# Kernel optimization log

Hardware: AMD Instinct MI355X
Metric: run time of the kernel (lower is better)

Reference implementation:

```python
import jax, jax.numpy as jnp
import numpy as np

TAU = 0.7
N_NODES = 1024
N_EDGES = 32768

def _mlp3(x, W1, b1, W2, b2, W3, b3):
    h = jax.nn.relu(x @ W1 + b1)
    h = jax.nn.relu(h @ W2 + b2)
    return h @ W3 + b3

def _gcn_conv(x, src, dst, W, b, n):
    # PyG GCNConv(add_self_loops=False): out = D^-1/2 A D^-1/2 (x W) + b
    deg = jax.ops.segment_sum(jnp.ones(src.shape[0], x.dtype), dst, num_segments=n)
    dinv = jnp.where(deg > 0, jax.lax.rsqrt(jnp.maximum(deg, 1.0)), 0.0)
    h = x @ W
    msg = h[src] * (dinv[src] * dinv[dst])[:, None]
    return jax.ops.segment_sum(msg, dst, num_segments=n) + b

def _forward(x1, x11, x2, mlp_W1, mlp_b1, mlp_W2, mlp_b2, mlp_W3, mlp_b3,
             m1_W1, m1_b1, m1_W2, m1_b2, m1_W3, m1_b3,
             wm1, bp1, bp2, wm12, wm13, class2,
             gcn1_W, gcn1_b, wm2, gcn2_W, gcn2_b, fc_W, fc_b, src, dst):
    n = x1.shape[0]
    logits = _mlp3(x1, mlp_W1, mlp_b1, mlp_W2, mlp_b2, mlp_W3, mlp_b3)  # [N,3]
    g = _mlp3(x11, m1_W1, m1_b1, m1_W2, m1_b2, m1_W3, m1_b3)            # [N,2]
    # hard argmax routing, softened: tau at argmax, (1-tau)/2 at the 2 others
    oh = jax.nn.one_hot(jnp.argmax(logits, axis=1), 3, dtype=logits.dtype)
    r = oh * TAU + (1.0 - oh) * ((1.0 - TAU) * 0.5)                     # [N,3]
    # fused form of: (einsum('nj,jkl',g,class2) * x2[...,None]).sum(-1) + g@b1
    res1 = jnp.einsum('nj,jkl,nk->nk', g, class2, x2) + g @ bp1         # [N,768]
    # fused form of: (einsum('nj,jkl',r,wm1) * res1[...,None]).sum(-1) + r@b2
    res1 = jnp.einsum('nj,jkl,nk->nk', r, wm1, res1) + r @ bp2          # [N,768]
    h1 = jax.nn.relu(_gcn_conv(res1, src, dst, gcn1_W, gcn1_b, n))      # [N,256]
    h1 = (r @ wm12) * h1 + 2e-4 * (res1 @ wm13)                         # [N,256]
    res2 = jnp.einsum('nj,jkl,nk->nk', r, wm2, h1)                      # [N,256]
    h2 = jax.nn.relu(_gcn_conv(res2, src, dst, gcn2_W, gcn2_b, n))      # [N,32]
    return jax.nn.log_softmax(h2 @ fc_W + fc_b, axis=1)                 # [N,8]

def setup_inputs():
    key = jax.random.key(0)
    ks = jax.random.split(key, 32)
    f = jnp.float32
    nrm = lambda i, s, sc=0.05: sc * jax.random.normal(ks[i], s, f)
    return {
        'x1': nrm(0, (N_NODES, 768), 1.0),
        'x11': nrm(1, (N_NODES, 768), 1.0),
        'x2': nrm(2, (N_NODES, 768), 1.0),
        'mlp_W1': nrm(3, (768, 512)), 'mlp_b1': jnp.zeros((512,), f),
        'mlp_W2': nrm(4, (512, 512)), 'mlp_b2': jnp.zeros((512,), f),
        'mlp_W3': nrm(5, (512, 3)), 'mlp_b3': jnp.zeros((3,), f),
        'm1_W1': nrm(6, (768, 512)), 'm1_b1': jnp.zeros((512,), f),
        'm1_W2': nrm(7, (512, 512)), 'm1_b2': jnp.zeros((512,), f),
        'm1_W3': nrm(8, (512, 2)), 'm1_b3': jnp.zeros((2,), f),
        'wm1': nrm(9, (3, 768, 256)),
        'bp1': jnp.zeros((2, 768), f),
        'bp2': jnp.zeros((3, 768), f),
        'wm12': jnp.ones((3, 256), f),
        'wm13': nrm(10, (768, 256)),
        'class2': jnp.ones((2, 768, 64), f),
        'gcn1_W': nrm(11, (768, 256)), 'gcn1_b': jnp.zeros((256,), f),
        'wm2': nrm(12, (3, 256, 256)),
        'gcn2_W': nrm(13, (256, 32)), 'gcn2_b': jnp.zeros((32,), f),
        'fc_W': nrm(14, (32, 8)), 'fc_b': jnp.zeros((8,), f),
        'edge_index': jax.random.randint(ks[15], (2, N_EDGES), 0, N_NODES),
    }

def reference(x1, x11, x2, mlp_W1, mlp_b1, mlp_W2, mlp_b2, mlp_W3, mlp_b3,
              m1_W1, m1_b1, m1_W2, m1_b2, m1_W3, m1_b3,
              wm1, bp1, bp2, wm12, wm13, class2,
              gcn1_W, gcn1_b, wm2, gcn2_W, gcn2_b, fc_W, fc_b, edge_index):
    src, dst = edge_index[0], edge_index[1]
    return _forward(x1, x11, x2, mlp_W1, mlp_b1, mlp_W2, mlp_b2, mlp_W3, mlp_b3,
                    m1_W1, m1_b1, m1_W2, m1_b2, m1_W3, m1_b3,
                    wm1, bp1, bp2, wm12, wm13, class2,
                    gcn1_W, gcn1_b, wm2, gcn2_W, gcn2_b, fc_W, fc_b, src, dst)
```

## Files before the change

kernel.cpp:

```cpp
#include <hip/hip_runtime.h>
#include <hip/hip_bf16.h>

#define NN 1024
#define NE 32768
#define TAU 0.7f
#define GAPT 0.01f

typedef __attribute__((ext_vector_type(8))) short short8;
typedef __attribute__((ext_vector_type(4))) float f32x4;

__device__ inline ushort bf16rne(float x) {
    union { float f; unsigned u; } a; a.f = x;
    unsigned r = (a.u + 0x7FFFu + ((a.u >> 16) & 1u)) >> 16;
    return (ushort)r;
}
__device__ inline float bf16tof(ushort h) {
    union { unsigned u; float f; } a; a.u = ((unsigned)h) << 16;
    return a.f;
}
__device__ inline void bf16split(float x, ushort& h, ushort& l) {
    h = bf16rne(x);
    l = bf16rne(x - bf16tof(h));
}

template <int K, int EPI>
__device__ __forceinline__ void gemm_wave(
    int lane, int rt, int ct,
    const ushort* __restrict__ Ah, const ushort* __restrict__ Al,
    const ushort* __restrict__ Bh, const ushort* __restrict__ Bl,
    const float* __restrict__ bias, const float* __restrict__ W3,
    float* __restrict__ Cf, ushort* __restrict__ Oh, ushort* __restrict__ Ol, int N) {
    int r0 = rt * 16, c0 = ct * 32;
    int g = lane >> 4, q = lane & 15;
    const ushort* pah = Ah + (size_t)(r0 + q) * K + g * 8;
    const ushort* pal = Al + (size_t)(r0 + q) * K + g * 8;
    const ushort* pb0h = Bh + (size_t)(c0 + q) * K + g * 8;
    const ushort* pb0l = Bl + (size_t)(c0 + q) * K + g * 8;
    const ushort* pb1h = pb0h + (size_t)16 * K;
    const ushort* pb1l = pb0l + (size_t)16 * K;
    f32x4 acc0 = {0.f, 0.f, 0.f, 0.f};
    f32x4 acc1 = {0.f, 0.f, 0.f, 0.f};
#pragma unroll 2
    for (int k0 = 0; k0 < K; k0 += 32) {
        short8 ah = *(const short8*)(pah + k0);
        short8 al = *(const short8*)(pal + k0);
        short8 b0h = *(const short8*)(pb0h + k0);
        short8 b0l = *(const short8*)(pb0l + k0);
        short8 b1h = *(const short8*)(pb1h + k0);
        short8 b1l = *(const short8*)(pb1l + k0);
        acc0 = __builtin_amdgcn_mfma_f32_16x16x32_bf16(ah, b0h, acc0, 0, 0, 0);
        acc1 = __builtin_amdgcn_mfma_f32_16x16x32_bf16(ah, b1h, acc1, 0, 0, 0);
        acc0 = __builtin_amdgcn_mfma_f32_16x16x32_bf16(ah, b0l, acc0, 0, 0, 0);
        acc1 = __builtin_amdgcn_mfma_f32_16x16x32_bf16(ah, b1l, acc1, 0, 0, 0);
        acc0 = __builtin_amdgcn_mfma_f32_16x16x32_bf16(al, b0h, acc0, 0, 0, 0);
        acc1 = __builtin_amdgcn_mfma_f32_16x16x32_bf16(al, b1h, acc1, 0, 0, 0);
    }
    int col0 = c0 + q, col1 = c0 + 16 + q;
    if constexpr (EPI == 0) {
#pragma unroll
        for (int i = 0; i < 4; i++) {
            int row = r0 + g * 4 + i;
            Cf[(size_t)row * N + col0] = acc0[i];
            Cf[(size_t)row * N + col1] = acc1[i];
        }
    } else if constexpr (EPI == 1) {
        float bv0 = bias[col0], bv1 = bias[col1];
#pragma unroll
        for (int i = 0; i < 4; i++) {
            int row = r0 + g * 4 + i;
            float a0 = fmaxf(acc0[i] + bv0, 0.f);
            float a1 = fmaxf(acc1[i] + bv1, 0.f);
            ushort h, l;
            bf16split(a0, h, l);
            Oh[(size_t)row * N + col0] = h;
            Ol[(size_t)row * N + col0] = l;
            bf16split(a1, h, l);
            Oh[(size_t)row * N + col1] = h;
            Ol[(size_t)row * N + col1] = l;
        }
    } else {
        constexpr int J = (EPI == 2) ? 3 : 2;
        constexpr int STR = (EPI == 2) ? 4 : 2;
        float bv0 = bias[col0], bv1 = bias[col1];
        float s[4][J];
#pragma unroll
        for (int i = 0; i < 4; i++) {
            float a0 = fmaxf(acc0[i] + bv0, 0.f);
            float a1 = fmaxf(acc1[i] + bv1, 0.f);
#pragma unroll
            for (int j = 0; j < J; j++)
                s[i][j] = a0 * W3[col0 * J + j] + a1 * W3[col1 * J + j];
        }
#pragma unroll
        for (int i = 0; i < 4; i++)
#pragma unroll
            for (int j = 0; j < J; j++) {
                float v = s[i][j];
#pragma unroll
                for (int m = 1; m < 16; m <<= 1) v += __shfl_xor(v, m);
                s[i][j] = v;
            }
        if (q == 0) {
#pragma unroll
            for (int i = 0; i < 4; i++) {
                int row = r0 + g * 4 + i;
#pragma unroll
                for (int j = 0; j < J; j++) atomicAdd(&Cf[(size_t)row * STR + j], s[i][j]);
            }
        }
    }
}

template <int M, int N, int K>
__global__ __launch_bounds__(256) void gemm3_n16(
    const ushort* __restrict__ Ah, const ushort* __restrict__ Al,
    const ushort* __restrict__ Bh, const ushort* __restrict__ Bl,
    float* __restrict__ Cf) {
    constexpr int RT = M / 16;
    constexpr int JOBS = RT * (N / 16);
    int wid = (blockIdx.x * 256 + threadIdx.x) >> 6;
    if (wid >= JOBS) return;
    int lane = threadIdx.x & 63;
    int rt = wid % RT, ct = wid / RT;
    int r0 = rt * 16, c0 = ct * 16;
    int g = lane >> 4, q = lane & 15;
    const ushort* pah = Ah + (size_t)(r0 + q) * K + g * 8;
    const ushort* pal = Al + (size_t)(r0 + q) * K + g * 8;
    const ushort* pbh = Bh + (size_t)(c0 + q) * K + g * 8;
    const ushort* pbl = Bl + (size_t)(c0 + q) * K + g * 8;
    f32x4 acc = {0.f, 0.f, 0.f, 0.f};
#pragma unroll 2
    for (int k0 = 0; k0 < K; k0 += 32) {
        short8 ah = *(const short8*)(pah + k0);
        short8 al = *(const short8*)(pal + k0);
        short8 bh = *(const short8*)(pbh + k0);
        short8 bl = *(const short8*)(pbl + k0);
        acc = __builtin_amdgcn_mfma_f32_16x16x32_bf16(ah, bh, acc, 0, 0, 0);
        acc = __builtin_amdgcn_mfma_f32_16x16x32_bf16(ah, bl, acc, 0, 0, 0);
        acc = __builtin_amdgcn_mfma_f32_16x16x32_bf16(al, bh, acc, 0, 0, 0);
    }
    int col = c0 + q;
#pragma unroll
    for (int i = 0; i < 4; i++) {
        int row = r0 + g * 4 + i;
        Cf[(size_t)row * N + col] = acc[i];
    }
}

template <int K, int EPI0, int EPI1, int RIDER>
__global__ __launch_bounds__(256) void gemm_pair(
    const ushort* __restrict__ Ah0, const ushort* __restrict__ Al0,
    const ushort* __restrict__ Bh0, const ushort* __restrict__ Bl0,
    const float* __restrict__ bias0, const float* __restrict__ W30,
    float* __restrict__ Cf0, ushort* __restrict__ Oh0, ushort* __restrict__ Ol0,
    const ushort* __restrict__ Ah1, const ushort* __restrict__ Al1,
    const ushort* __restrict__ Bh1, const ushort* __restrict__ Bl1,
    const float* __restrict__ bias1, const float* __restrict__ W31,
    float* __restrict__ Cf1, ushort* __restrict__ Oh1, ushort* __restrict__ Ol1,
    const int* __restrict__ esrc, const int* __restrict__ edst,
    const int* __restrict__ part, int* __restrict__ rowst, int* __restrict__ cursor,
    float* __restrict__ dinv, int* __restrict__ adj) {
    if (RIDER == 1 && blockIdx.x >= 512) {
        __shared__ int ps[256];
        int t = threadIdx.x;
        int d0 = 0, d1 = 0, d2 = 0, d3 = 0;
#pragma unroll
        for (int b = 0; b < 8; b++) {
            int4 qv = *(const int4*)(part + b * 1024 + t * 4);
            d0 += qv.x; d1 += qv.y; d2 += qv.z; d3 += qv.w;
        }
        int sum = d0 + d1 + d2 + d3;
        ps[t] = sum;
        __syncthreads();
        for (int off = 1; off < 256; off <<= 1) {
            int v = (t >= off) ? ps[t - off] : 0;
            __syncthreads();
            ps[t] += v;
            __syncthreads();
        }
        int r0 = ps[t] - sum;
        int r1 = r0 + d0, r2 = r1 + d1, r3 = r2 + d2;
        rowst[t * 4 + 0] = r0;
        rowst[t * 4 + 1] = r1;
        rowst[t * 4 + 2] = r2;
        rowst[t * 4 + 3] = r3;
        if (t == 255) rowst[1024] = r3 + d3;
        cursor[t * 4 + 0] = r0;
        cursor[t * 4 + 1] = r1;
        cursor[t * 4 + 2] = r2;
        cursor[t * 4 + 3] = r3;
        dinv[t * 4 + 0] = d0 > 0 ? rsqrtf((float)d0) : 0.f;
        dinv[t * 4 + 1] = d1 > 0 ? rsqrtf((float)d1) : 0.f;
        dinv[t * 4 + 2] = d2 > 0 ? rsqrtf((float)d2) : 0.f;
        dinv[t * 4 + 3] = d3 > 0 ? rsqrtf((float)d3) : 0.f;
        return;
    }
    if (RIDER == 2 && blockIdx.x >= 512) {
        int e = (blockIdx.x - 512) * 256 + threadIdx.x;
        int d = edst[e];
        int slot = atomicAdd(&cursor[d], 1);
        adj[slot] = esrc[e];
        return;
    }
    int wid = (blockIdx.x * 256 + threadIdx.x) >> 6;
    int lane = threadIdx.x & 63;
    int pair = wid >> 10;
    int widl = wid & 1023;
    int rt = widl & 63, ct = widl >> 6;
    if (pair == 0)
        gemm_wave<K, EPI0>(lane, rt, ct, Ah0, Al0, Bh0, Bl0, bias0, W30, Cf0, Oh0, Ol0, 512);
    else
        gemm_wave<K, EPI1>(lane, rt, ct, Ah1, Al1, Bh1, Bl1, bias1, W31, Cf1, Oh1, Ol1, 512);
}

__device__ void dev_zero(int sub, int t, float* zbase) {
    for (int i = sub * 256 + t; i < 6144; i += 512) zbase[i] = 0.f;
}

__device__ void dev_tabs_wave(int gw, int lane, const float* __restrict__ class2,
                              const float* __restrict__ wm1, const float* __restrict__ wm2,
                              float* __restrict__ C2s, float* __restrict__ Wm1s,
                              float* __restrict__ Wm2s) {
    if (gw < 2304) {
        float4 v = *(const float4*)(wm1 + (size_t)gw * 256 + lane * 4);
        float s = v.x + v.y + v.z + v.w;
#pragma unroll
        for (int m = 32; m; m >>= 1) s += __shfl_xor(s, m);
        if (lane == 0) Wm1s[gw] = s;
    } else if (gw < 3072) {
        int j = gw - 2304;
        float4 v = *(const float4*)(wm2 + (size_t)j * 256 + lane * 4);
        float s = v.x + v.y + v.z + v.w;
#pragma unroll
        for (int m = 32; m; m >>= 1) s += __shfl_xor(s, m);
        if (lane == 0) Wm2s[j] = s;
    } else {
        int row = (gw - 3072) * 4 + (lane >> 4);
        float4 v = *(const float4*)(class2 + (size_t)row * 64 + (lane & 15) * 4);
        float s = v.x + v.y + v.z + v.w;
#pragma unroll
        for (int m = 8; m; m >>= 1) s += __shfl_xor(s, m);
        if ((lane & 15) == 0) C2s[row] = s;
    }
}

__device__ void dev_splitx(int sub, int t, const float* __restrict__ X,
                           ushort* __restrict__ Xh, ushort* __restrict__ Xl) {
    int j = sub * 256 + t;
    float4 v = ((const float4*)X)[j];
    ushort h0, l0, h1, l1, h2, l2, h3, l3;
    bf16split(v.x, h0, l0);
    bf16split(v.y, h1, l1);
    bf16split(v.z, h2, l2);
    bf16split(v.w, h3, l3);
    ((ushort4*)Xh)[j] = make_ushort4(h0, h1, h2, h3);
    ((ushort4*)Xl)[j] = make_ushort4(l0, l1, l2, l3);
}

__global__ __launch_bounds__(1024) void aux0(
    const float* class2, const float* wm1, const float* wm2,
    float* C2s, float* Wm1s, float* Wm2s, float* zbase,
    const float* x1, ushort* XH1, ushort* XL1,
    const float* x11, ushort* XH2, ushort* XL2,
    const float* W1a, ushort* W1AH, ushort* W1AL,
    const float* W1b, ushort* W1BH, ushort* W1BL,
    const float* W2a, ushort* W2AH, ushort* W2AL,
    const float* W2b, ushort* W2BH, ushort* W2BL,
    const float* G1W, ushort* GWH, ushort* GWL,
    const float* W13, const int* edst, int* part) {
    if (blockIdx.x >= 1017) {
        __shared__ int hist[1024];
        int b = blockIdx.x - 1017;
        int t = threadIdx.x;
        hist[t] = 0;
        __syncthreads();
        const int* ep = edst + b * 4096;
#pragma unroll
        for (int i = 0; i < 4; i++) atomicAdd(&hist[ep[t + i * 1024]], 1);
        __syncthreads();
        part[b * 1024 + t] = hist[t];
        return;
    }
    __shared__ float tb[4][32][33];
    int quad = threadIdx.x >> 8;
    int t = threadIdx.x & 255;
    int sub = blockIdx.x * 4 + quad;
    if (sub >= 4066) return;
    const float* W = nullptr;
    ushort *Th = nullptr, *Tl = nullptr;
    int K = 0, N = 0, tile = 0;
    if (sub >= 3874)      { W = W13; Th = GWH + 256 * 768; Tl = GWL + 256 * 768; K = 768; N = 256; tile = sub - 3874; }
    else if (sub >= 3682) { W = G1W; Th = GWH; Tl = GWL; K = 768; N = 256; tile = sub - 3682; }
    else if (sub >= 3426) { W = W2b; Th = W2BH; Tl = W2BL; K = 512; N = 512; tile = sub - 3426; }
    else if (sub >= 3170) { W = W2a; Th = W2AH; Tl = W2AL; K = 512; N = 512; tile = sub - 3170; }
    else if (sub >= 2786) { W = W1b; Th = W1BH; Tl = W1BL; K = 768; N = 512; tile = sub - 2786; }
    else if (sub >= 2402) { W = W1a; Th = W1AH; Tl = W1AL; K = 768; N = 512; tile = sub - 2402; }
    int k0 = 0, n0 = 0;
    if (W) {
        k0 = (tile % (K / 32)) * 32;
        n0 = (tile / (K / 32)) * 32;
        int tx = t % 32, ty = t / 32;
        for (int i = ty; i < 32; i += 8)
            tb[quad][i][tx] = W[(size_t)(k0 + i) * N + n0 + tx];
    } else if (sub < 2) dev_zero(sub, t, zbase);
    else if (sub < 866) dev_tabs_wave((sub - 2) * 4 + (t >> 6), t & 63,
                                      class2, wm1, wm2, C2s, Wm1s, Wm2s);
    else if (sub < 1634) dev_splitx(sub - 866, t, x1, XH1, XL1);
    else dev_splitx(sub - 1634, t, x11, XH2, XL2);
    __syncthreads();
    if (W) {
        int tx = t % 32, ty = t / 32;
        for (int i = ty; i < 32; i += 8) {
            float v = tb[quad][tx][i];
            ushort h, l;
            bf16split(v, h, l);
            Th[(size_t)(n0 + i) * K + k0 + tx] = h;
            Tl[(size_t)(n0 + i) * K + k0 + tx] = l;
        }
    }
}

__global__ __launch_bounds__(256) void finrep(
    const float* __restrict__ LG, const float* __restrict__ b3, float* __restrict__ rbuf,
    const float* __restrict__ x1, const float* __restrict__ W1, const float* __restrict__ b1,
    const float* __restrict__ W2, const float* __restrict__ b2, const float* __restrict__ W3) {
    __shared__ int snode[4];
    __shared__ int scnt;
    __shared__ float part[4][512];
    __shared__ float xs[768];
    __shared__ float h1[512];
    __shared__ float h2[512];
    int t = threadIdx.x;
    if (t == 0) scnt = 0;
    __syncthreads();
    if (t < 4) {
        int n = blockIdx.x * 4 + t;
        float l0 = LG[n * 4 + 0] + b3[0];
        float l1 = LG[n * 4 + 1] + b3[1];
        float l2 = LG[n * 4 + 2] + b3[2];
        int am = 0;
        float mv = l0;
        if (l1 > mv) { mv = l1; am = 1; }
        if (l2 > mv) { mv = l2; am = 2; }
        float sec = (am == 0) ? fmaxf(l1, l2) : ((am == 1) ? fmaxf(l0, l2) : fmaxf(l0, l1));
        float lo = (1.f - TAU) * 0.5f;
        rbuf[n * 4 + 0] = (am == 0) ? TAU : lo;
        rbuf[n * 4 + 1] = (am == 1) ? TAU : lo;
        rbuf[n * 4 + 2] = (am == 2) ? TAU : lo;
        if (mv - sec < GAPT) {
            int s = atomicAdd(&scnt, 1);
            snode[s] = n;
        }
    }
    __syncthreads();
    int cnt = scnt;
    int w = t >> 6, l = t & 63;
    for (int it = 0; it < cnt; it++) {
        int n = snode[it];
        for (int k = t; k < 768; k += 256) xs[k] = x1[(size_t)n * 768 + k];
        __syncthreads();
        {
            float acc[8] = {0.f, 0.f, 0.f, 0.f, 0.f, 0.f, 0.f, 0.f};
            for (int k = w * 192; k < (w + 1) * 192; k++) {
                float xv = xs[k];
                const float* wr = W1 + (size_t)k * 512 + l;
#pragma unroll
                for (int c = 0; c < 8; c++) acc[c] += xv * wr[64 * c];
            }
#pragma unroll
            for (int c = 0; c < 8; c++) part[w][l + 64 * c] = acc[c];
        }
        __syncthreads();
        for (int d = t; d < 512; d += 256)
            h1[d] = fmaxf(part[0][d] + part[1][d] + part[2][d] + part[3][d] + b1[d], 0.f);
        __syncthreads();
        {
            float acc[8] = {0.f, 0.f, 0.f, 0.f, 0.f, 0.f, 0.f, 0.f};
            for (int k = w * 128; k < (w + 1) * 128; k++) {
                float xv = h1[k];
                const float* wr = W2 + (size_t)k * 512 + l;
#pragma unroll
                for (int c = 0; c < 8; c++) acc[c] += xv * wr[64 * c];
            }
#pragma unroll
            for (int c = 0; c < 8; c++) part[w][l + 64 * c] = acc[c];
        }
        __syncthreads();
        for (int d = t; d < 512; d += 256)
            h2[d] = fmaxf(part[0][d] + part[1][d] + part[2][d] + part[3][d] + b2[d], 0.f);
        __syncthreads();
        if (t < 64) {
            float p0 = 0.f, p1 = 0.f, p2 = 0.f;
            for (int k = t; k < 512; k += 64) {
                float hv = h2[k];
                p0 += hv * W3[k * 3 + 0];
                p1 += hv * W3[k * 3 + 1];
                p2 += hv * W3[k * 3 + 2];
            }
            for (int off = 32; off; off >>= 1) {
                p0 += __shfl_down(p0, off);
                p1 += __shfl_down(p1, off);
                p2 += __shfl_down(p2, off);
            }
            if (t == 0) {
                float l0 = p0 + b3[0], l1 = p1 + b3[1], l2 = p2 + b3[2];
                int am = 0;
                float mv = l0;
                if (l1 > mv) { mv = l1; am = 1; }
                if (l2 > mv) { mv = l2; am = 2; }
                float lo = (1.f - TAU) * 0.5f;
                rbuf[n * 4 + 0] = (am == 0) ? TAU : lo;
                rbuf[n * 4 + 1] = (am == 1) ? TAU : lo;
                rbuf[n * 4 + 2] = (am == 2) ? TAU : lo;
            }
        }
        __syncthreads();
    }
}

__global__ __launch_bounds__(256) void res1_kernel(
    const float* __restrict__ x2, const float* __restrict__ G, const float* __restrict__ m1b3,
    const float* __restrict__ rbuf, const float* __restrict__ C2s, const float* __restrict__ bp1,
    const float* __restrict__ Wm1s, const float* __restrict__ bp2,
    ushort* __restrict__ r1h, ushort* __restrict__ r1l) {
    int idx = blockIdx.x * 256 + threadIdx.x;
    int n = idx / 192;
    int kq = (idx % 192) * 4;
    float g0 = G[n * 2 + 0] + m1b3[0], g1 = G[n * 2 + 1] + m1b3[1];
    float r0 = rbuf[n * 4 + 0], r1 = rbuf[n * 4 + 1], r2 = rbuf[n * 4 + 2];
    float4 xv = *(const float4*)(x2 + (size_t)n * 768 + kq);
    float4 c0 = *(const float4*)(C2s + kq);
    float4 c1 = *(const float4*)(C2s + 768 + kq);
    float4 p0 = *(const float4*)(bp1 + kq);
    float4 p1 = *(const float4*)(bp1 + 768 + kq);
    float4 w0 = *(const float4*)(Wm1s + kq);
    float4 w1 = *(const float4*)(Wm1s + 768 + kq);
    float4 w2 = *(const float4*)(Wm1s + 1536 + kq);
    float4 q0 = *(const float4*)(bp2 + kq);
    float4 q1 = *(const float4*)(bp2 + 768 + kq);
    float4 q2 = *(const float4*)(bp2 + 1536 + kq);
    float o[4];
    o[0] = (xv.x * (g0 * c0.x + g1 * c1.x) + g0 * p0.x + g1 * p1.x) * (r0 * w0.x + r1 * w1.x + r2 * w2.x) + r0 * q0.x + r1 * q1.x + r2 * q2.x;
    o[1] = (xv.y * (g0 * c0.y + g1 * c1.y) + g0 * p0.y + g1 * p1.y) * (r0 * w0.y + r1 * w1.y + r2 * w2.y) + r0 * q0.y + r1 * q1.y + r2 * q2.y;
    o[2] = (xv.z * (g0 * c0.z + g1 * c1.z) + g0 * p0.z + g1 * p1.z) * (r0 * w0.z + r1 * w1.z + r2 * w2.z) + r0 * q0.z + r1 * q1.z + r2 * q2.z;
    o[3] = (xv.w * (g0 * c0.w + g1 * c1.w) + g0 * p0.w + g1 * p1.w) * (r0 * w0.w + r1 * w1.w + r2 * w2.w) + r0 * q0.w + r1 * q1.w + r2 * q2.w;
    ushort h[4], l[4];
#pragma unroll
    for (int i = 0; i < 4; i++) bf16split(o[i], h[i], l[i]);
    size_t off = ((size_t)n * 768 + kq) / 4;
    ((ushort4*)r1h)[off] = make_ushort4(h[0], h[1], h[2], h[3]);
    ((ushort4*)r1l)[off] = make_ushort4(l[0], l[1], l[2], l[3]);
}

__global__ __launch_bounds__(256) void gather1_combine(
    const float* __restrict__ gcw, const int* __restrict__ rowst, const int* __restrict__ adj,
    const float* __restrict__ dinv, const float* __restrict__ gcn1_b,
    const float* __restrict__ rbuf, const float* __restrict__ wm12,
    const float* __restrict__ Wm2s, float* __restrict__ res2f) {
    int n = blockIdx.x;
    int k = threadIdx.x;
    int lane = threadIdx.x & 63;
    int e0 = rowst[n], e1 = rowst[n + 1];
    float acc = 0.f;
    for (int base = e0; base < e1; base += 64) {
        int idx = base + lane;
        int s_i = 0;
        float w_i = 0.f;
        if (idx < e1) { s_i = adj[idx]; w_i = dinv[s_i]; }
        int mm = min(64, e1 - base);
        for (int j = 0; j < mm; j++) {
            int s = __shfl(s_i, j);
            float w = __shfl(w_i, j);
            acc += gcw[(size_t)s * 512 + k] * w;
        }
    }
    float h1 = dinv[n] * acc + gcn1_b[k];
    float mv = gcw[(size_t)n * 512 + 256 + k];
    float r0 = rbuf[n * 4 + 0], r1 = rbuf[n * 4 + 1], r2 = rbuf[n * 4 + 2];
    float a = r0 * wm12[k] + r1 * wm12[256 + k] + r2 * wm12[512 + k];
    float w = r0 * Wm2s[k] + r1 * Wm2s[256 + k] + r2 * Wm2s[512 + k];
    res2f[(size_t)n * 256 + k] = w * (a * fmaxf(h1, 0.f) + 2e-4f * mv);
}

__global__ __launch_bounds__(256) void gather2_full(
    const float* __restrict__ res2f, const int* __restrict__ rowst,
    const int* __restrict__ adj, const float* __restrict__ dinv,
    const float* __restrict__ G2W, const float* __restrict__ gcn2_b,
    const float* __restrict__ fcW, const float* __restrict__ fcb,
    float* __restrict__ out) {
    __shared__ float gres[256];
    __shared__ float part[8][32];
    int t = threadIdx.x;
    int lane = t & 63;
    int n = blockIdx.x;
    int e0 = rowst[n], e1 = rowst[n + 1];
    float acc = 0.f;
    for (int base = e0; base < e1; base += 64) {
        int idx = base + lane;
        int s_i = 0;
        float w_i = 0.f;
        if (idx < e1) { s_i = adj[idx]; w_i = dinv[s_i]; }
        int mm = min(64, e1 - base);
        for (int j = 0; j < mm; j++) {
            int s = __shfl(s_i, j);
            float w = __shfl(w_i, j);
            acc += res2f[(size_t)s * 256 + t] * w;
        }
    }
    gres[t] = acc * dinv[n];
    __syncthreads();
    int j = t & 31, seg = t >> 5;
    float p = 0.f;
#pragma unroll
    for (int kk = 0; kk < 32; kk++) {
        int k = seg * 32 + kk;
        p += gres[k] * G2W[k * 32 + j];
    }
    part[seg][j] = p;
    __syncthreads();
    if (t < 32) {
        float h2 = part[0][t] + part[1][t] + part[2][t] + part[3][t] +
                   part[4][t] + part[5][t] + part[6][t] + part[7][t] + gcn2_b[t];
        gres[t] = fmaxf(h2, 0.f);
    }
    __syncthreads();
    if (t < 8) {
        float logit = fcb[t];
#pragma unroll
        for (int i = 0; i < 32; i++) logit += gres[i] * fcW[i * 8 + t];
        float m = logit;
        for (int off = 4; off; off >>= 1) m = fmaxf(m, __shfl_xor(m, off, 8));
        float e = expf(logit - m), s = e;
        for (int off = 4; off; off >>= 1) s += __shfl_xor(s, off, 8);
        out[(size_t)n * 8 + t] = logit - m - logf(s);
    }
}

extern "C" void kernel_launch(void* const* d_in, const int* in_sizes, int n_in,
                              void* d_out, int out_size, void* d_ws, size_t ws_size,
                              hipStream_t stream) {
    const float* x1     = (const float*)d_in[0];
    const float* x11    = (const float*)d_in[1];
    const float* x2     = (const float*)d_in[2];
    const float* mlp_W1 = (const float*)d_in[3];
    const float* mlp_b1 = (const float*)d_in[4];
    const float* mlp_W2 = (const float*)d_in[5];
    const float* mlp_b2 = (const float*)d_in[6];
    const float* mlp_W3 = (const float*)d_in[7];
    const float* mlp_b3 = (const float*)d_in[8];
    const float* m1_W1  = (const float*)d_in[9];
    const float* m1_b1  = (const float*)d_in[10];
    const float* m1_W2  = (const float*)d_in[11];
    const float* m1_b2  = (const float*)d_in[12];
    const float* m1_W3  = (const float*)d_in[13];
    const float* m1_b3  = (const float*)d_in[14];
    const float* wm1    = (const float*)d_in[15];
    const float* bp1    = (const float*)d_in[16];
    const float* bp2    = (const float*)d_in[17];
    const float* wm12   = (const float*)d_in[18];
    const float* wm13   = (const float*)d_in[19];
    const float* class2 = (const float*)d_in[20];
    const float* gcn1_W = (const float*)d_in[21];
    const float* gcn1_b = (const float*)d_in[22];
    const float* wm2    = (const float*)d_in[23];
    const float* gcn2_W = (const float*)d_in[24];
    const float* gcn2_b = (const float*)d_in[25];
    const float* fc_W   = (const float*)d_in[26];
    const float* fc_b   = (const float*)d_in[27];
    const int* eidx     = (const int*)d_in[28];
    const int* esrc = eidx;
    const int* edst = eidx + NE;

    char* ws = (char*)d_ws;
    ushort* XH1   = (ushort*)(ws + 0x0000000);
    ushort* XL1   = (ushort*)(ws + 0x0180000);
    ushort* XH2   = (ushort*)(ws + 0x0300000);
    ushort* XL2   = (ushort*)(ws + 0x0480000);
    ushort* W1AH  = (ushort*)(ws + 0x0600000);
    ushort* W1AL  = (ushort*)(ws + 0x06C0000);
    ushort* W1BH  = (ushort*)(ws + 0x0780000);
    ushort* W1BL  = (ushort*)(ws + 0x0840000);
    ushort* W2AH  = (ushort*)(ws + 0x0900000);
    ushort* W2AL  = (ushort*)(ws + 0x0980000);
    ushort* W2BH  = (ushort*)(ws + 0x0A00000);
    ushort* W2BL  = (ushort*)(ws + 0x0A80000);
    ushort* GWH   = (ushort*)(ws + 0x0B00000);
    ushort* GWL   = (ushort*)(ws + 0x0BC0000);
    ushort* HS1AH = (ushort*)(ws + 0x0D00000);
    ushort* HS1AL = (ushort*)(ws + 0x0E00000);
    ushort* HS1BH = (ushort*)(ws + 0x0F00000);
    ushort* HS1BL = (ushort*)(ws + 0x1000000);
    ushort* RES1H = (ushort*)(ws + 0x1100000);
    ushort* RES1L = (ushort*)(ws + 0x1280000);
    float*  GCW   = (float*)(ws + 0x1400000);
    float*  RES2F = (float*)(ws + 0x1600000);
    float* LOGITS = (float*)(ws + 0x1740000);
    float* GBUF   = (float*)(ws + 0x1744000);
    float* RBUF   = (float*)(ws + 0x1746000);
    float* DINV   = (float*)(ws + 0x174A000);
    int*   ROWST  = (int*)(ws + 0x174B000);
    int*   CURS   = (int*)(ws + 0x174D000);
    int*   ADJ    = (int*)(ws + 0x174E000);
    int*   PART   = (int*)(ws + 0x1780000);
    float* C2S    = (float*)(ws + 0x1770000);
    float* WM1S   = (float*)(ws + 0x1772000);
    float* WM2S   = (float*)(ws + 0x1775000);

    aux0<<<1025, 1024, 0, stream>>>(class2, wm1, wm2, C2S, WM1S, WM2S, LOGITS,
                                    x1, XH1, XL1, x11, XH2, XL2,
                                    mlp_W1, W1AH, W1AL, m1_W1, W1BH, W1BL,
                                    mlp_W2, W2AH, W2AL, m1_W2, W2BH, W2BL,
                                    gcn1_W, GWH, GWL, wm13, edst, PART);
    gemm_pair<768, 1, 1, 1><<<513, 256, 0, stream>>>(
        XH1, XL1, W1AH, W1AL, mlp_b1, nullptr, nullptr, HS1AH, HS1AL,
        XH2, XL2, W1BH, W1BL, m1_b1, nullptr, nullptr, HS1BH, HS1BL,
        esrc, edst, PART, ROWST, CURS, DINV, ADJ);
    gemm_pair<512, 2, 3, 2><<<640, 256, 0, stream>>>(
        HS1AH, HS1AL, W2AH, W2AL, mlp_b2, mlp_W3, LOGITS, nullptr, nullptr,
        HS1BH, HS1BL, W2BH, W2BL, m1_b2, m1_W3, GBUF, nullptr, nullptr,
        esrc, edst, PART, ROWST, CURS, DINV, ADJ);
    finrep<<<256, 256, 0, stream>>>(LOGITS, mlp_b3, RBUF, x1, mlp_W1, mlp_b1,
                                    mlp_W2, mlp_b2, mlp_W3);
    res1_kernel<<<768, 256, 0, stream>>>(x2, GBUF, m1_b3, RBUF, C2S, bp1, WM1S, bp2,
                                         RES1H, RES1L);
    gemm3_n16<1024, 512, 768><<<512, 256, 0, stream>>>(RES1H, RES1L, GWH, GWL, GCW);
    gather1_combine<<<NN, 256, 0, stream>>>(GCW, ROWST, ADJ, DINV, gcn1_b, RBUF,
                                            wm12, WM2S, RES2F);
    gather2_full<<<NN, 256, 0, stream>>>(RES2F, ROWST, ADJ, DINV, gcn2_W, gcn2_b,
                                         fc_W, fc_b, (float*)d_out);
}
```

Measured before the change: 165.4 us.

## Fuse tail stages into one cooperative kernel with grid-wide syncs

The four tail launches (res1, the split-bf16 GEMM, and the two GCN gathers) become one cooperative persistent kernel whose phases are separated by grid syncs. The goal is to remove per-launch overhead and the idle gaps between the dependent small kernels. In exchange, the GEMM phase is a simpler per-wave MFMA loop that reads operands straight from global memory instead of the templated gemm3_n16, and the grid is capped by occupancy, which could leave parallelism unused. The old launch sequence stays as a fallback if the cooperative launch fails.

```diff
diff --git a/kernel.cpp b/kernel.cpp
--- a/kernel.cpp
+++ b/kernel.cpp
@@ -1,5 +1,8 @@
 #include <hip/hip_runtime.h>
 #include <hip/hip_bf16.h>
+#include <hip/hip_cooperative_groups.h>
+
+namespace cg = cooperative_groups;
 
 #define NN 1024
 #define NE 32768
@@ -418,12 +421,12 @@
     }
 }
 
-__global__ __launch_bounds__(256) void res1_kernel(
-    const float* __restrict__ x2, const float* __restrict__ G, const float* __restrict__ m1b3,
-    const float* __restrict__ rbuf, const float* __restrict__ C2s, const float* __restrict__ bp1,
+__device__ __forceinline__ void res1_body(
+    int idx, const float* __restrict__ x2, const float* __restrict__ G,
+    const float* __restrict__ m1b3, const float* __restrict__ rbuf,
+    const float* __restrict__ C2s, const float* __restrict__ bp1,
     const float* __restrict__ Wm1s, const float* __restrict__ bp2,
     ushort* __restrict__ r1h, ushort* __restrict__ r1l) {
-    int idx = blockIdx.x * 256 + threadIdx.x;
     int n = idx / 192;
     int kq = (idx % 192) * 4;
     float g0 = G[n * 2 + 0] + m1b3[0], g1 = G[n * 2 + 1] + m1b3[1];
@@ -444,22 +447,30 @@
     o[1] = (xv.y * (g0 * c0.y + g1 * c1.y) + g0 * p0.y + g1 * p1.y) * (r0 * w0.y + r1 * w1.y + r2 * w2.y) + r0 * q0.y + r1 * q1.y + r2 * q2.y;
     o[2] = (xv.z * (g0 * c0.z + g1 * c1.z) + g0 * p0.z + g1 * p1.z) * (r0 * w0.z + r1 * w1.z + r2 * w2.z) + r0 * q0.z + r1 * q1.z + r2 * q2.z;
     o[3] = (xv.w * (g0 * c0.w + g1 * c1.w) + g0 * p0.w + g1 * p1.w) * (r0 * w0.w + r1 * w1.w + r2 * w2.w) + r0 * q0.w + r1 * q1.w + r2 * q2.w;
-    ushort h[4], l[4];
-#pragma unroll
-    for (int i = 0; i < 4; i++) bf16split(o[i], h[i], l[i]);
+    ushort hh[4], ll[4];
+#pragma unroll
+    for (int i = 0; i < 4; i++) bf16split(o[i], hh[i], ll[i]);
     size_t off = ((size_t)n * 768 + kq) / 4;
-    ((ushort4*)r1h)[off] = make_ushort4(h[0], h[1], h[2], h[3]);
-    ((ushort4*)r1l)[off] = make_ushort4(l[0], l[1], l[2], l[3]);
-}
-
-__global__ __launch_bounds__(256) void gather1_combine(
-    const float* __restrict__ gcw, const int* __restrict__ rowst, const int* __restrict__ adj,
-    const float* __restrict__ dinv, const float* __restrict__ gcn1_b,
-    const float* __restrict__ rbuf, const float* __restrict__ wm12,
-    const float* __restrict__ Wm2s, float* __restrict__ res2f) {
-    int n = blockIdx.x;
-    int k = threadIdx.x;
-    int lane = threadIdx.x & 63;
+    ((ushort4*)r1h)[off] = make_ushort4(hh[0], hh[1], hh[2], hh[3]);
+    ((ushort4*)r1l)[off] = make_ushort4(ll[0], ll[1], ll[2], ll[3]);
+}
+
+__global__ __launch_bounds__(256) void res1_kernel(
+    const float* __restrict__ x2, const float* __restrict__ G, const float* __restrict__ m1b3,
+    const float* __restrict__ rbuf, const float* __restrict__ C2s, const float* __restrict__ bp1,
+    const float* __restrict__ Wm1s, const float* __restrict__ bp2,
+    ushort* __restrict__ r1h, ushort* __restrict__ r1l) {
+    res1_body(blockIdx.x * 256 + threadIdx.x, x2, G, m1b3, rbuf, C2s, bp1, Wm1s, bp2, r1h, r1l);
+}
+
+__device__ __forceinline__ void gather1_body(
+    int n, int t, const float* __restrict__ gcw, const int* __restrict__ rowst,
+    const int* __restrict__ adj, const float* __restrict__ dinv,
+    const float* __restrict__ gcn1_b, const float* __restrict__ rbuf,
+    const float* __restrict__ wm12, const float* __restrict__ Wm2s,
+    float* __restrict__ res2f) {
+    int k = t;
+    int lane = t & 63;
     int e0 = rowst[n], e1 = rowst[n + 1];
     float acc = 0.f;
     for (int base = e0; base < e1; base += 64) {
@@ -474,25 +485,30 @@
             acc += gcw[(size_t)s * 512 + k] * w;
         }
     }
-    float h1 = dinv[n] * acc + gcn1_b[k];
+    float h1v = dinv[n] * acc + gcn1_b[k];
     float mv = gcw[(size_t)n * 512 + 256 + k];
     float r0 = rbuf[n * 4 + 0], r1 = rbuf[n * 4 + 1], r2 = rbuf[n * 4 + 2];
     float a = r0 * wm12[k] + r1 * wm12[256 + k] + r2 * wm12[512 + k];
     float w = r0 * Wm2s[k] + r1 * Wm2s[256 + k] + r2 * Wm2s[512 + k];
-    res2f[(size_t)n * 256 + k] = w * (a * fmaxf(h1, 0.f) + 2e-4f * mv);
-}
-
-__global__ __launch_bounds__(256) void gather2_full(
+    res2f[(size_t)n * 256 + k] = w * (a * fmaxf(h1v, 0.f) + 2e-4f * mv);
+}
+
+__global__ __launch_bounds__(256) void gather1_combine(
+    const float* __restrict__ gcw, const int* __restrict__ rowst, const int* __restrict__ adj,
+    const float* __restrict__ dinv, const float* __restrict__ gcn1_b,
+    const float* __restrict__ rbuf, const float* __restrict__ wm12,
+    const float* __restrict__ Wm2s, float* __restrict__ res2f) {
+    gather1_body(blockIdx.x, threadIdx.x, gcw, rowst, adj, dinv, gcn1_b, rbuf, wm12, Wm2s, res2f);
+}
+
+__device__ __forceinline__ void gather2_body(
+    int n, int t, float* gres, float (*part)[32],
     const float* __restrict__ res2f, const int* __restrict__ rowst,
     const int* __restrict__ adj, const float* __restrict__ dinv,
     const float* __restrict__ G2W, const float* __restrict__ gcn2_b,
     const float* __restrict__ fcW, const float* __restrict__ fcb,
     float* __restrict__ out) {
-    __shared__ float gres[256];
-    __shared__ float part[8][32];
-    int t = threadIdx.x;
     int lane = t & 63;
-    int n = blockIdx.x;
     int e0 = rowst[n], e1 = rowst[n + 1];
     float acc = 0.f;
     for (int base = e0; base < e1; base += 64) {
@@ -519,9 +535,9 @@
     part[seg][j] = p;
     __syncthreads();
     if (t < 32) {
-        float h2 = part[0][t] + part[1][t] + part[2][t] + part[3][t] +
-                   part[4][t] + part[5][t] + part[6][t] + part[7][t] + gcn2_b[t];
-        gres[t] = fmaxf(h2, 0.f);
+        float h2v = part[0][t] + part[1][t] + part[2][t] + part[3][t] +
+                    part[4][t] + part[5][t] + part[6][t] + part[7][t] + gcn2_b[t];
+        gres[t] = fmaxf(h2v, 0.f);
     }
     __syncthreads();
     if (t < 8) {
@@ -533,6 +549,84 @@
         float e = expf(logit - m), s = e;
         for (int off = 4; off; off >>= 1) s += __shfl_xor(s, off, 8);
         out[(size_t)n * 8 + t] = logit - m - logf(s);
+    }
+    __syncthreads();
+}
+
+__global__ __launch_bounds__(256) void gather2_full(
+    const float* __restrict__ res2f, const int* __restrict__ rowst,
+    const int* __restrict__ adj, const float* __restrict__ dinv,
+    const float* __restrict__ G2W, const float* __restrict__ gcn2_b,
+    const float* __restrict__ fcW, const float* __restrict__ fcb,
+    float* __restrict__ out) {
+    __shared__ float gres[256];
+    __shared__ float part[8][32];
+    gather2_body(blockIdx.x, threadIdx.x, gres, part, res2f, rowst, adj, dinv,
+                 G2W, gcn2_b, fcW, fcb, out);
+}
+
+__global__ __launch_bounds__(256) void tail_coop(
+    const float* __restrict__ x2, const float* __restrict__ G, const float* __restrict__ m1b3,
+    const float* __restrict__ rbuf, const float* __restrict__ C2s, const float* __restrict__ bp1,
+    const float* __restrict__ Wm1s, const float* __restrict__ bp2,
+    ushort* __restrict__ r1h, ushort* __restrict__ r1l,
+    const ushort* __restrict__ GWH, const ushort* __restrict__ GWL,
+    float* __restrict__ gcw,
+    const int* __restrict__ rowst, const int* __restrict__ adj, const float* __restrict__ dinv,
+    const float* __restrict__ gcn1_b, const float* __restrict__ wm12,
+    const float* __restrict__ Wm2s, float* __restrict__ res2f,
+    const float* __restrict__ G2W, const float* __restrict__ gcn2_b,
+    const float* __restrict__ fcW, const float* __restrict__ fcb, float* __restrict__ out) {
+    cg::grid_group gg = cg::this_grid();
+    int t = threadIdx.x;
+    int nthreads = gridDim.x * 256;
+
+    for (int idx = blockIdx.x * 256 + t; idx < 196608; idx += nthreads)
+        res1_body(idx, x2, G, m1b3, rbuf, C2s, bp1, Wm1s, bp2, r1h, r1l);
+    gg.sync();
+
+    {
+        int totwaves = gridDim.x * 4;
+        int lane = t & 63;
+        for (int wid = (blockIdx.x * 256 + t) >> 6; wid < 2048; wid += totwaves) {
+            constexpr int K = 768, Nn = 512;
+            int rt = wid & 63, ct = wid >> 6;
+            int r0 = rt * 16, c0 = ct * 16;
+            int g = lane >> 4, q = lane & 15;
+            const ushort* pah = r1h + (size_t)(r0 + q) * K + g * 8;
+            const ushort* pal = r1l + (size_t)(r0 + q) * K + g * 8;
+            const ushort* pbh = GWH + (size_t)(c0 + q) * K + g * 8;
+            const ushort* pbl = GWL + (size_t)(c0 + q) * K + g * 8;
+            f32x4 acc = {0.f, 0.f, 0.f, 0.f};
+#pragma unroll 2
+            for (int k0 = 0; k0 < K; k0 += 32) {
+                short8 ah = *(const short8*)(pah + k0);
+                short8 al = *(const short8*)(pal + k0);
+                short8 bh = *(const short8*)(pbh + k0);
+                short8 bl = *(const short8*)(pbl + k0);
+                acc = __builtin_amdgcn_mfma_f32_16x16x32_bf16(ah, bh, acc, 0, 0, 0);
+                acc = __builtin_amdgcn_mfma_f32_16x16x32_bf16(ah, bl, acc, 0, 0, 0);
+                acc = __builtin_amdgcn_mfma_f32_16x16x32_bf16(al, bh, acc, 0, 0, 0);
+            }
+            int col = c0 + q;
+#pragma unroll
+            for (int i = 0; i < 4; i++) {
+                int row = r0 + g * 4 + i;
+                gcw[(size_t)row * Nn + col] = acc[i];
+            }
+        }
+    }
+    gg.sync();
+
+    for (int n = blockIdx.x; n < NN; n += gridDim.x)
+        gather1_body(n, t, gcw, rowst, adj, dinv, gcn1_b, rbuf, wm12, Wm2s, res2f);
+    gg.sync();
+
+    {
+        __shared__ float gres[256];
+        __shared__ float part[8][32];
+        for (int n = blockIdx.x; n < NN; n += gridDim.x)
+            gather2_body(n, t, gres, part, res2f, rowst, adj, dinv, G2W, gcn2_b, fcW, fcb, out);
     }
 }
 
@@ -601,10 +695,10 @@
     int*   ROWST  = (int*)(ws + 0x174B000);
     int*   CURS   = (int*)(ws + 0x174D000);
     int*   ADJ    = (int*)(ws + 0x174E000);
-    int*   PART   = (int*)(ws + 0x1780000);
     float* C2S    = (float*)(ws + 0x1770000);
     float* WM1S   = (float*)(ws + 0x1772000);
     float* WM2S   = (float*)(ws + 0x1775000);
+    int*   PART   = (int*)(ws + 0x1780000);
 
     aux0<<<1025, 1024, 0, stream>>>(class2, wm1, wm2, C2S, WM1S, WM2S, LOGITS,
                                     x1, XH1, XL1, x11, XH2, XL2,
@@ -621,11 +715,31 @@
         esrc, edst, PART, ROWST, CURS, DINV, ADJ);
     finrep<<<256, 256, 0, stream>>>(LOGITS, mlp_b3, RBUF, x1, mlp_W1, mlp_b1,
                                     mlp_W2, mlp_b2, mlp_W3);
-    res1_kernel<<<768, 256, 0, stream>>>(x2, GBUF, m1_b3, RBUF, C2S, bp1, WM1S, bp2,
-                                         RES1H, RES1L);
-    gemm3_n16<1024, 512, 768><<<512, 256, 0, stream>>>(RES1H, RES1L, GWH, GWL, GCW);
-    gather1_combine<<<NN, 256, 0, stream>>>(GCW, ROWST, ADJ, DINV, gcn1_b, RBUF,
-                                            wm12, WM2S, RES2F);
-    gather2_full<<<NN, 256, 0, stream>>>(RES2F, ROWST, ADJ, DINV, gcn2_W, gcn2_b,
-                                         fc_W, fc_b, (float*)d_out);
-}
+
+    hipError_t lerr = hipErrorUnknown;
+    int occ = 0;
+    if (hipOccupancyMaxActiveBlocksPerMultiprocessor(&occ, tail_coop, 256, 0) == hipSuccess &&
+        occ >= 1) {
+        int nb = occ * 256;
+        if (nb > 1024) nb = 1024;
+        float* outp = (float*)d_out;
+        const float* m1b3p = m1_b3;
+        void* args[] = {
+            (void*)&x2, (void*)&GBUF, (void*)&m1b3p, (void*)&RBUF, (void*)&C2S,
+            (void*)&bp1, (void*)&WM1S, (void*)&bp2, (void*)&RES1H, (void*)&RES1L,
+            (void*)&GWH, (void*)&GWL, (void*)&GCW, (void*)&ROWST, (void*)&ADJ,
+            (void*)&DINV, (void*)&gcn1_b, (void*)&wm12, (void*)&WM2S, (void*)&RES2F,
+            (void*)&gcn2_W, (void*)&gcn2_b, (void*)&fc_W, (void*)&fc_b, (void*)&outp};
+        lerr = hipLaunchCooperativeKernel((const void*)tail_coop, dim3(nb), dim3(256),
+                                          args, 0, stream);
+    }
+    if (lerr != hipSuccess) {
+        res1_kernel<<<768, 256, 0, stream>>>(x2, GBUF, m1_b3, RBUF, C2S, bp1, WM1S, bp2,
+                                             RES1H, RES1L);
+        gemm3_n16<1024, 512, 768><<<512, 256, 0, stream>>>(RES1H, RES1L, GWH, GWL, GCW);
+        gather1_combine<<<NN, 256, 0, stream>>>(GCW, ROWST, ADJ, DINV, gcn1_b, RBUF,
+                                                wm12, WM2S, RES2F);
+        gather2_full<<<NN, 256, 0, stream>>>(RES2F, ROWST, ADJ, DINV, gcn2_W, gcn2_b,
+                                             fc_W, fc_b, (float*)d_out);
+    }
+}
```

After: 345.0 us. 109% more time.
